# Kernel optimization log

Hardware: AMD Instinct MI355X
Metric: run time of the kernel (lower is better)

The kernel has to match this reference:

```python
import jax, jax.numpy as jnp
import numpy as np

N = 50000      # nodes
E = 800000     # edges (avg degree 16)
IN_DIM = 128
H = 4          # attention heads
D = 32         # hidden dim per head
NEG_SLOPE = 0.2


def setup_inputs() -> dict:
    key = jax.random.key(0)
    ks = jax.random.split(key, 9)
    x = jax.random.normal(ks[0], (N, IN_DIM), dtype=jnp.float32)
    src = jax.random.randint(ks[1], (E,), 0, N, dtype=jnp.int64)
    dst = jax.random.randint(ks[2], (E,), 0, N, dtype=jnp.int64)
    # layer 0: IN_DIM -> H*D ; layer 1: H*D -> H*D
    s0 = 1.0 / np.sqrt(IN_DIM)
    s1 = 1.0 / np.sqrt(H * D)
    W1 = jax.random.normal(ks[3], (H * D, IN_DIM), dtype=jnp.float32) * s0
    al1 = jax.random.normal(ks[4], (1, H, D), dtype=jnp.float32) * s1
    ar1 = jax.random.normal(ks[5], (1, H, D), dtype=jnp.float32) * s1
    W2 = jax.random.normal(ks[6], (H * D, H * D), dtype=jnp.float32) * s1
    al2 = jax.random.normal(ks[7], (1, H, D), dtype=jnp.float32) * s1
    ar2 = jax.random.normal(ks[8], (1, H, D), dtype=jnp.float32) * s1
    return {"x": x, "src": src, "dst": dst, "W1": W1, "al1": al1, "ar1": ar1,
            "W2": W2, "al2": al2, "ar2": ar2}


def gat_conv(h, src, dst, W, al, ar):
    """DGL-style GATConv. h: [N, F_in] -> [N, H, D], with ELU activation."""
    feat = (h @ W.T).reshape(N, H, D)                 # [N,H,D]
    el = jnp.sum(feat * al, axis=-1)                  # [N,H] a_l . Wh
    er = jnp.sum(feat * ar, axis=-1)                  # [N,H] a_r . Wh
    e = jax.nn.leaky_relu(el[src] + er[dst], NEG_SLOPE)  # [E,H]
    # numerically stable edge softmax over incoming edges of each dst node
    m = jax.ops.segment_max(e, dst, num_segments=N)   # [N,H]
    ee = jnp.exp(e - m[dst])                          # [E,H]
    denom = jax.ops.segment_sum(ee, dst, num_segments=N)  # [N,H]
    alpha = ee / denom[dst]                           # [E,H]
    msg = feat[src] * alpha[..., None]                # [E,H,D]
    out = jax.ops.segment_sum(msg, dst, num_segments=N)   # [N,H,D]
    return jax.nn.elu(out)


def reference(x, src, dst, W1, al1, ar1, W2, al2, ar2):
    h = gat_conv(x, src, dst, W1, al1, ar1).reshape(N, H * D)  # flatten(1)
    h = gat_conv(h, src, dst, W2, al2, ar2)                    # [N,H,D]
    return jnp.mean(h, axis=1)                                 # [N,D]
```

## Files before the change

### kernel.cpp

```cpp
#include <hip/hip_runtime.h>
#include <cmath>
#include <type_traits>

#define HEADS 4
#define FDIM 128
#define NEG 0.2f
#define NBUCK 8

typedef __attribute__((ext_vector_type(8))) __bf16 bf16x8;
typedef __attribute__((ext_vector_type(8))) _Float16 h16x8;
typedef __attribute__((ext_vector_type(4))) float f32x4;

__global__ __launch_bounds__(256) void prep_kernel(
    const float* __restrict__ W1, const float* __restrict__ al1,
    const float* __restrict__ ar1,
    const float* __restrict__ W2, const float* __restrict__ al2,
    const float* __restrict__ ar2,
    __bf16* __restrict__ wf1, __bf16* __restrict__ wext1,
    __bf16* __restrict__ wf2, __bf16* __restrict__ wext2)
{
    const int b = blockIdx.x, tid = threadIdx.x;
    if (b < 256) {
        const float* W = (b < 128) ? W1 : W2;
        __bf16* wf = (b < 128) ? wf1 : wf2;
        int idx = (b & 127) * 256 + tid;
        int j = idx & 7;
        int r = idx >> 3;
        int c = r & 15; r >>= 4;
        int t = r & 7;  r >>= 3;
        int kq = r & 15;
        int hl = r >> 4;
        float v = W[(t * 16 + c) * 128 + kq * 8 + j];
        __bf16 hi = (__bf16)v;
        wf[idx] = (hl == 0) ? hi : (__bf16)(v - (float)hi);
    } else {
        const float* W  = (b == 256) ? W1 : W2;
        const float* al = (b == 256) ? al1 : al2;
        const float* ar = (b == 256) ? ar1 : ar2;
        __bf16* wext = (b == 256) ? wext1 : wext2;
        __shared__ float val[1024];
        #pragma unroll
        for (int ch = 0; ch < 4; ++ch) {
            int idx = ch * 256 + tid;
            int c = idx >> 7, k = idx & 127;
            int h = c & 3;
            const float* a = (c < 4) ? al : ar;
            float s = 0.f;
            for (int d = 0; d < 32; ++d)
                s += a[h * 32 + d] * W[(h * 32 + d) * 128 + k];
            val[c * 128 + k] = s;
        }
        __syncthreads();
        #pragma unroll
        for (int ch = 0; ch < 16; ++ch) {
            int idx = tid * 16 + ch;
            int j = idx & 7;
            int r = idx >> 3;
            int c = r & 15; r >>= 4;
            int kq = r & 15;
            int hl = r >> 4;
            float v = (c < 8) ? val[c * 128 + kq * 8 + j] : 0.f;
            __bf16 hi = (__bf16)v;
            wext[idx] = (hl == 0) ? hi : (__bf16)(v - (float)hi);
        }
    }
}

template <typename XT>
__global__ __launch_bounds__(256) void gemm_mfma_kernel(
    const XT* __restrict__ X, const bf16x8* __restrict__ wf,
    const bf16x8* __restrict__ wext,
    _Float16* __restrict__ featH,
    float* __restrict__ el, float* __restrict__ er,
    int nnodes, int ntiles)
{
    __shared__ bf16x8 lw[4096];
    const int tid = threadIdx.x;
    for (int i = tid; i < 4096; i += 256) lw[i] = wf[i];
    __syncthreads();

    const int wave = tid >> 6, lane = tid & 63;
    const int l15 = lane & 15, quad = lane >> 4;

    int tile = blockIdx.x;
    float xr[32], xn[32];

    auto loadX = [&](int tl, float* dst) {
        int nodeA = tl * 64 + wave * 16 + l15;
        bool v = nodeA < nnodes;
        if constexpr (std::is_same<XT, float>::value) {
            const float4* xp = (const float4*)(X + (size_t)nodeA * 128);
            #pragma unroll
            for (int ks = 0; ks < 4; ++ks) {
                float4 a = v ? xp[ks * 8 + quad * 2]     : make_float4(0.f, 0.f, 0.f, 0.f);
                float4 b = v ? xp[ks * 8 + quad * 2 + 1] : make_float4(0.f, 0.f, 0.f, 0.f);
                dst[ks * 8 + 0] = a.x; dst[ks * 8 + 1] = a.y;
                dst[ks * 8 + 2] = a.z; dst[ks * 8 + 3] = a.w;
                dst[ks * 8 + 4] = b.x; dst[ks * 8 + 5] = b.y;
                dst[ks * 8 + 6] = b.z; dst[ks * 8 + 7] = b.w;
            }
        } else {
            const h16x8* xp = (const h16x8*)(X + (size_t)nodeA * 128);
            #pragma unroll
            for (int ks = 0; ks < 4; ++ks) {
                h16x8 hv;
                if (v) {
                    hv = xp[ks * 4 + quad];
                } else {
                    #pragma unroll
                    for (int j = 0; j < 8; ++j) hv[j] = (_Float16)0.f;
                }
                #pragma unroll
                for (int j = 0; j < 8; ++j) dst[ks * 8 + j] = (float)hv[j];
            }
        }
    };

    loadX(tile, xr);
    while (true) {
        int next = tile + gridDim.x;
        if (next < ntiles) loadX(next, xn);

        f32x4 acc[9];
        #pragma unroll
        for (int t = 0; t < 9; ++t) acc[t] = (f32x4){0.f, 0.f, 0.f, 0.f};

        #pragma unroll
        for (int ks = 0; ks < 4; ++ks) {
            bf16x8 ahi, alo;
            #pragma unroll
            for (int j = 0; j < 8; ++j) {
                float xv = xr[ks * 8 + j];
                __bf16 h = (__bf16)xv;
                ahi[j] = h;
                alo[j] = (__bf16)(xv - (float)h);
            }
            const int kq = ks * 4 + quad;

            {
                bf16x8 bh = wext[(kq) * 16 + l15];
                bf16x8 bl = wext[(16 + kq) * 16 + l15];
                acc[8] = __builtin_amdgcn_mfma_f32_16x16x32_bf16(ahi, bh, acc[8], 0, 0, 0);
                acc[8] = __builtin_amdgcn_mfma_f32_16x16x32_bf16(alo, bh, acc[8], 0, 0, 0);
                acc[8] = __builtin_amdgcn_mfma_f32_16x16x32_bf16(ahi, bl, acc[8], 0, 0, 0);
            }
            #pragma unroll
            for (int t = 0; t < 8; ++t) {
                bf16x8 bh = lw[(kq * 8 + t) * 16 + l15];
                bf16x8 bl = lw[((16 + kq) * 8 + t) * 16 + l15];
                acc[t] = __builtin_amdgcn_mfma_f32_16x16x32_bf16(ahi, bh, acc[t], 0, 0, 0);
                acc[t] = __builtin_amdgcn_mfma_f32_16x16x32_bf16(alo, bh, acc[t], 0, 0, 0);
                acc[t] = __builtin_amdgcn_mfma_f32_16x16x32_bf16(ahi, bl, acc[t], 0, 0, 0);
            }
        }

        const int nodeC = tile * 64 + wave * 16 + quad * 4;
        #pragma unroll
        for (int r = 0; r < 4; ++r) {
            int gn = nodeC + r;
            if (gn < nnodes) {
                #pragma unroll
                for (int t = 0; t < 8; ++t)
                    featH[(size_t)gn * 128 + t * 16 + l15] = (_Float16)acc[t][r];
            }
        }
        if (l15 < 8) {
            #pragma unroll
            for (int r = 0; r < 4; ++r) {
                int gn = nodeC + r;
                if (gn < nnodes) {
                    if (l15 < 4) el[gn * HEADS + l15] = acc[8][r];
                    else         er[gn * HEADS + (l15 - 4)] = acc[8][r];
                }
            }
        }

        if (next >= ntiles) break;
        #pragma unroll
        for (int i = 0; i < 32; ++i) xr[i] = xn[i];
        tile = next;
    }
}

__global__ __launch_bounds__(256) void hist_kernel(
    const int* __restrict__ src, const int* __restrict__ dst,
    int* __restrict__ counts, int* __restrict__ rank, int nedges, int shift)
{
    int i0 = (blockIdx.x * 256 + threadIdx.x) * 4;
    if (i0 + 3 < nedges) {
        int4 d = *(const int4*)&dst[i0];
        int4 s = *(const int4*)&src[i0];
        int4 r;
        r.x = atomicAdd(&counts[d.x * NBUCK + (s.x >> shift)], 1);
        r.y = atomicAdd(&counts[d.y * NBUCK + (s.y >> shift)], 1);
        r.z = atomicAdd(&counts[d.z * NBUCK + (s.z >> shift)], 1);
        r.w = atomicAdd(&counts[d.w * NBUCK + (s.w >> shift)], 1);
        *(int4*)&rank[i0] = r;
    } else {
        for (int i = i0; i < nedges; ++i)
            rank[i] = atomicAdd(&counts[dst[i] * NBUCK + (src[i] >> shift)], 1);
    }
}

__global__ __launch_bounds__(256) void scan1_kernel(
    const int* __restrict__ counts, int* __restrict__ offsets,
    int* __restrict__ bsums, int n)
{
    __shared__ int wsums[4];
    const int tid = threadIdx.x, lane = tid & 63, w = tid >> 6;
    const int i = blockIdx.x * 1024 + tid * 4;

    int4 v = make_int4(0, 0, 0, 0);
    if (i + 3 < n) v = *(const int4*)&counts[i];
    else {
        if (i < n)     v.x = counts[i];
        if (i + 1 < n) v.y = counts[i + 1];
        if (i + 2 < n) v.z = counts[i + 2];
    }
    int s0 = v.x, s1 = s0 + v.y, s2 = s1 + v.z, s3 = s2 + v.w;

    int x = s3;
    #pragma unroll
    for (int off = 1; off < 64; off <<= 1) {
        int t = __shfl_up(x, off, 64);
        if (lane >= off) x += t;
    }
    if (lane == 63) wsums[w] = x;
    __syncthreads();
    int wbase = 0;
    #pragma unroll
    for (int k = 0; k < 4; ++k) if (k < w) wbase += wsums[k];

    int tbase = wbase + x - s3;
    if (i < n)     offsets[i]     = tbase;
    if (i + 1 < n) offsets[i + 1] = tbase + s0;
    if (i + 2 < n) offsets[i + 2] = tbase + s1;
    if (i + 3 < n) offsets[i + 3] = tbase + s2;
    if (tid == 255) bsums[blockIdx.x] = wbase + x;
}

__global__ __launch_bounds__(64) void scan2_kernel(int* __restrict__ bsums, int nb)
{
    const int lane = threadIdx.x;
    int run = 0;
    for (int base = 0; base < nb; base += 64) {
        int i = base + lane;
        int v = (i < nb) ? bsums[i] : 0;
        int x = v;
        #pragma unroll
        for (int off = 1; off < 64; off <<= 1) {
            int t = __shfl_up(x, off, 64);
            if (lane >= off) x += t;
        }
        if (i < nb) bsums[i] = run + x - v;
        run += __shfl(x, 63, 64);
    }
}

__global__ __launch_bounds__(256) void scan3_kernel(
    int* __restrict__ offsets, const int* __restrict__ bsums, int n, int nedges)
{
    const int i = blockIdx.x * 1024 + threadIdx.x * 4;
    const int base = bsums[blockIdx.x];
    #pragma unroll
    for (int k = 0; k < 4; ++k)
        if (i + k < n) offsets[i + k] += base;
    if (blockIdx.x == 0 && threadIdx.x == 0) offsets[n] = nedges;
}

__global__ __launch_bounds__(256) void scatter_kernel(
    const int* __restrict__ src, const int* __restrict__ dst,
    const int* __restrict__ rank, const int* __restrict__ offsets,
    int* __restrict__ csr_src, int nedges, int shift)
{
    int i0 = (blockIdx.x * 256 + threadIdx.x) * 4;
    if (i0 + 3 < nedges) {
        int4 d = *(const int4*)&dst[i0];
        int4 r = *(const int4*)&rank[i0];
        int4 s = *(const int4*)&src[i0];
        csr_src[offsets[d.x * NBUCK + (s.x >> shift)] + r.x] = s.x;
        csr_src[offsets[d.y * NBUCK + (s.y >> shift)] + r.y] = s.y;
        csr_src[offsets[d.z * NBUCK + (s.z >> shift)] + r.z] = s.z;
        csr_src[offsets[d.w * NBUCK + (s.w >> shift)] + r.w] = s.w;
    } else {
        for (int i = i0; i < nedges; ++i)
            csr_src[offsets[dst[i] * NBUCK + (src[i] >> shift)] + rank[i]] = src[i];
    }
}

template <bool MEAN>
__global__ __launch_bounds__(256) void aggregate_kernel(
    const _Float16* __restrict__ featH, const float* __restrict__ el,
    const float* __restrict__ er, const int* __restrict__ offsets,
    const int* __restrict__ csr_src, void* __restrict__ outp, int nnodes)
{
    const int wid = (blockIdx.x * 256 + threadIdx.x) >> 6;
    const int lane = threadIdx.x & 63;
    const int g = lane >> 4, u = lane & 15, h = u >> 2;
    const int n = wid * 4 + g;
    const bool nv = n < nnodes;

    int beg = 0, end = 0;
    float ern = 0.f;
    if (nv) {
        beg = offsets[n * NBUCK];
        end = offsets[n * NBUCK + NBUCK];
        ern = er[n * HEADS + h];
    }
    int md = end - beg;
    md = max(md, __shfl_xor(md, 16, 64));
    md = max(md, __shfl_xor(md, 32, 64));

    float a[8];
    #pragma unroll
    for (int p = 0; p < 8; ++p) a[p] = 0.f;
    float sw = 0.f;

    int j = beg;
    bool v = j < end;
    int s = v ? csr_src[j] : 0;
    float q = el[s * HEADS + h];
    h16x8 f = ((const h16x8*)(featH + (size_t)s * 128))[u];

    for (int it = 0; it < md; ++it) {
        int jn = j + 1;
        bool vn = jn < end;
        int sn = vn ? csr_src[jn] : 0;
        float qn = el[sn * HEADS + h];
        h16x8 fn = ((const h16x8*)(featH + (size_t)sn * 128))[u];

        float e = q + ern;
        e = e > 0.f ? e : NEG * e;
        float w = v ? __expf(e) : 0.f;
        #pragma unroll
        for (int p = 0; p < 8; ++p) a[p] += w * (float)f[p];
        sw += w;

        j = jn; v = vn; q = qn; f = fn;
    }

    float inv = sw > 0.f ? 1.f / sw : 0.f;
    float r[8];
    #pragma unroll
    for (int p = 0; p < 8; ++p) {
        float t = a[p] * inv;
        r[p] = t > 0.f ? t : expm1f(t);
    }

    if (!MEAN) {
        if (nv) {
            h16x8 o;
            #pragma unroll
            for (int p = 0; p < 8; ++p) o[p] = (_Float16)r[p];
            ((h16x8*)outp)[(size_t)n * 16 + u] = o;
        }
    } else {
        #pragma unroll
        for (int p = 0; p < 8; ++p) {
            r[p] += __shfl_xor(r[p], 4, 64);
            r[p] += __shfl_xor(r[p], 8, 64);
        }
        if (nv && u < 4) {
            float* out = (float*)outp;
            float4* o4 = (float4*)(out + (size_t)n * 32 + u * 8);
            o4[0] = make_float4(0.25f * r[0], 0.25f * r[1], 0.25f * r[2], 0.25f * r[3]);
            o4[1] = make_float4(0.25f * r[4], 0.25f * r[5], 0.25f * r[6], 0.25f * r[7]);
        }
    }
}

extern "C" void kernel_launch(void* const* d_in, const int* in_sizes, int n_in,
                              void* d_out, int out_size, void* d_ws, size_t ws_size,
                              hipStream_t stream)
{
    const float* x   = (const float*)d_in[0];
    const int*   src = (const int*)d_in[1];
    const int*   dst = (const int*)d_in[2];
    const float* W1  = (const float*)d_in[3];
    const float* al1 = (const float*)d_in[4];
    const float* ar1 = (const float*)d_in[5];
    const float* W2  = (const float*)d_in[6];
    const float* al2 = (const float*)d_in[7];
    const float* ar2 = (const float*)d_in[8];

    const int N = in_sizes[0] / FDIM;
    const int E = in_sizes[1];
    const int NB = N * NBUCK;

    int shift = 0;
    while (((N - 1) >> shift) > (NBUCK - 1)) ++shift;

    _Float16* h1 = (_Float16*)d_ws;
    _Float16* featH = h1 + (size_t)N * FDIM;
    float* el = (float*)(featH + (size_t)N * FDIM);
    float* er = el + (size_t)N * HEADS;
    int* counts  = (int*)(er + (size_t)N * HEADS);
    int* offsets = counts + NB;
    int* rank    = offsets + (NB + 1);
    int* csr_src = rank + E;
    int* bsums   = csr_src + E;
    uintptr_t wp = ((uintptr_t)(bsums + 512) + 63) & ~(uintptr_t)63;
    __bf16* wf1   = (__bf16*)wp;
    __bf16* wext1 = wf1 + 32768;
    __bf16* wf2   = wext1 + 4096;
    __bf16* wext2 = wf2 + 32768;

    const int ntiles = (N + 63) / 64;
    const int gemm_grid = ntiles < 256 ? ntiles : 256;
    const int edge4_grid = ((E + 3) / 4 + 255) / 256;
    const int agg_grid  = ((N + 3) / 4 + 3) / 4;
    const int nscan     = (NB + 1023) / 1024;

    prep_kernel<<<258, 256, 0, stream>>>(W1, al1, ar1, W2, al2, ar2,
                                         wf1, wext1, wf2, wext2);

    (void)hipMemsetAsync(counts, 0, (size_t)NB * sizeof(int), stream);
    hist_kernel<<<edge4_grid, 256, 0, stream>>>(src, dst, counts, rank, E, shift);
    scan1_kernel<<<nscan, 256, 0, stream>>>(counts, offsets, bsums, NB);
    scan2_kernel<<<1, 64, 0, stream>>>(bsums, nscan);
    scan3_kernel<<<nscan, 256, 0, stream>>>(offsets, bsums, NB, E);
    scatter_kernel<<<edge4_grid, 256, 0, stream>>>(src, dst, rank, offsets,
                                                   csr_src, E, shift);

    gemm_mfma_kernel<float><<<gemm_grid, 256, 0, stream>>>(
        x, (const bf16x8*)wf1, (const bf16x8*)wext1, featH, el, er, N, ntiles);
    aggregate_kernel<false><<<agg_grid, 256, 0, stream>>>(
        featH, el, er, offsets, csr_src, (void*)h1, N);

    gemm_mfma_kernel<_Float16><<<gemm_grid, 256, 0, stream>>>(
        h1, (const bf16x8*)wf2, (const bf16x8*)wext2, featH, el, er, N, ntiles);
    aggregate_kernel<true><<<agg_grid, 256, 0, stream>>>(
        featH, el, er, offsets, csr_src, d_out, N);
}
```

Baseline: 250.0 us.

## Split each node's edges across a wave, fuse memset and scan stages

The aggregate kernel now assigns one 64-lane wave per destination node. Its four 16-lane groups stride over the node's edges and combine partial sums with cross-lane shuffles, where previously each group handled its own node for as many iterations as the longest of the four. Zeroing the histogram counts is folded into extra prep_kernel blocks in place of a memset. The single-block scan2 and scan3 kernels are merged so that each block sums the preceding block totals itself. The intent is to remove load imbalance from varying degrees and cut two launches, at the cost of four times as many aggregate waves and extra shuffle reductions.

```diff
diff --git a/kernel.cpp b/kernel.cpp
--- a/kernel.cpp
+++ b/kernel.cpp
@@ -17,7 +17,8 @@
     const float* __restrict__ W2, const float* __restrict__ al2,
     const float* __restrict__ ar2,
     __bf16* __restrict__ wf1, __bf16* __restrict__ wext1,
-    __bf16* __restrict__ wf2, __bf16* __restrict__ wext2)
+    __bf16* __restrict__ wf2, __bf16* __restrict__ wext2,
+    int* __restrict__ counts, int nb)
 {
     const int b = blockIdx.x, tid = threadIdx.x;
     if (b < 256) {
@@ -33,7 +34,7 @@
         float v = W[(t * 16 + c) * 128 + kq * 8 + j];
         __bf16 hi = (__bf16)v;
         wf[idx] = (hl == 0) ? hi : (__bf16)(v - (float)hi);
-    } else {
+    } else if (b < 258) {
         const float* W  = (b == 256) ? W1 : W2;
         const float* al = (b == 256) ? al1 : al2;
         const float* ar = (b == 256) ? ar1 : ar2;
@@ -62,6 +63,13 @@
             float v = (c < 8) ? val[c * 128 + kq * 8 + j] : 0.f;
             __bf16 hi = (__bf16)v;
             wext[idx] = (hl == 0) ? hi : (__bf16)(v - (float)hi);
+        }
+    } else {
+        int i0 = ((b - 258) * 256 + tid) * 4;
+        if (i0 + 3 < nb) {
+            *(int4*)&counts[i0] = make_int4(0, 0, 0, 0);
+        } else {
+            for (int i = i0; i < nb; ++i) counts[i] = 0;
         }
     }
 }
@@ -239,33 +247,25 @@
     if (tid == 255) bsums[blockIdx.x] = wbase + x;
 }
 
-__global__ __launch_bounds__(64) void scan2_kernel(int* __restrict__ bsums, int nb)
-{
-    const int lane = threadIdx.x;
-    int run = 0;
-    for (int base = 0; base < nb; base += 64) {
-        int i = base + lane;
-        int v = (i < nb) ? bsums[i] : 0;
-        int x = v;
-        #pragma unroll
-        for (int off = 1; off < 64; off <<= 1) {
-            int t = __shfl_up(x, off, 64);
-            if (lane >= off) x += t;
-        }
-        if (i < nb) bsums[i] = run + x - v;
-        run += __shfl(x, 63, 64);
-    }
-}
-
-__global__ __launch_bounds__(256) void scan3_kernel(
+__global__ __launch_bounds__(256) void scan23_kernel(
     int* __restrict__ offsets, const int* __restrict__ bsums, int n, int nedges)
 {
-    const int i = blockIdx.x * 1024 + threadIdx.x * 4;
-    const int base = bsums[blockIdx.x];
+    __shared__ int sbase;
+    const int tid = threadIdx.x, b = blockIdx.x;
+    if (tid < 64) {
+        int s = 0;
+        for (int i = tid; i < b; i += 64) s += bsums[i];
+        #pragma unroll
+        for (int off = 1; off < 64; off <<= 1) s += __shfl_xor(s, off, 64);
+        if (tid == 0) sbase = s;
+    }
+    __syncthreads();
+    const int base = sbase;
+    const int i = b * 1024 + tid * 4;
     #pragma unroll
     for (int k = 0; k < 4; ++k)
         if (i + k < n) offsets[i + k] += base;
-    if (blockIdx.x == 0 && threadIdx.x == 0) offsets[n] = nedges;
+    if (b == 0 && tid == 0) offsets[n] = nedges;
 }
 
 __global__ __launch_bounds__(256) void scatter_kernel(
@@ -294,36 +294,27 @@
     const float* __restrict__ er, const int* __restrict__ offsets,
     const int* __restrict__ csr_src, void* __restrict__ outp, int nnodes)
 {
-    const int wid = (blockIdx.x * 256 + threadIdx.x) >> 6;
+    const int n = (blockIdx.x * 256 + threadIdx.x) >> 6;
+    if (n >= nnodes) return;
     const int lane = threadIdx.x & 63;
     const int g = lane >> 4, u = lane & 15, h = u >> 2;
-    const int n = wid * 4 + g;
-    const bool nv = n < nnodes;
-
-    int beg = 0, end = 0;
-    float ern = 0.f;
-    if (nv) {
-        beg = offsets[n * NBUCK];
-        end = offsets[n * NBUCK + NBUCK];
-        ern = er[n * HEADS + h];
-    }
-    int md = end - beg;
-    md = max(md, __shfl_xor(md, 16, 64));
-    md = max(md, __shfl_xor(md, 32, 64));
+    const int beg = offsets[n * NBUCK], end = offsets[n * NBUCK + NBUCK];
+    const float ern = er[n * HEADS + h];
+    const int iters = (end - beg + 3) >> 2;
 
     float a[8];
     #pragma unroll
     for (int p = 0; p < 8; ++p) a[p] = 0.f;
     float sw = 0.f;
 
-    int j = beg;
+    int j = beg + g;
     bool v = j < end;
     int s = v ? csr_src[j] : 0;
     float q = el[s * HEADS + h];
     h16x8 f = ((const h16x8*)(featH + (size_t)s * 128))[u];
 
-    for (int it = 0; it < md; ++it) {
-        int jn = j + 1;
+    for (int it = 0; it < iters; ++it) {
+        int jn = j + 4;
         bool vn = jn < end;
         int sn = vn ? csr_src[jn] : 0;
         float qn = el[sn * HEADS + h];
@@ -339,6 +330,14 @@
         j = jn; v = vn; q = qn; f = fn;
     }
 
+    #pragma unroll
+    for (int p = 0; p < 8; ++p) {
+        a[p] += __shfl_xor(a[p], 16, 64);
+        a[p] += __shfl_xor(a[p], 32, 64);
+    }
+    sw += __shfl_xor(sw, 16, 64);
+    sw += __shfl_xor(sw, 32, 64);
+
     float inv = sw > 0.f ? 1.f / sw : 0.f;
     float r[8];
     #pragma unroll
@@ -348,7 +347,7 @@
     }
 
     if (!MEAN) {
-        if (nv) {
+        if (g == 0) {
             h16x8 o;
             #pragma unroll
             for (int p = 0; p < 8; ++p) o[p] = (_Float16)r[p];
@@ -360,7 +359,7 @@
             r[p] += __shfl_xor(r[p], 4, 64);
             r[p] += __shfl_xor(r[p], 8, 64);
         }
-        if (nv && u < 4) {
+        if (g == 0 && u < 4) {
             float* out = (float*)outp;
             float4* o4 = (float4*)(out + (size_t)n * 32 + u * 8);
             o4[0] = make_float4(0.25f * r[0], 0.25f * r[1], 0.25f * r[2], 0.25f * r[3]);
@@ -408,17 +407,16 @@
     const int ntiles = (N + 63) / 64;
     const int gemm_grid = ntiles < 256 ? ntiles : 256;
     const int edge4_grid = ((E + 3) / 4 + 255) / 256;
-    const int agg_grid  = ((N + 3) / 4 + 3) / 4;
+    const int agg_grid  = (N + 3) / 4;
     const int nscan     = (NB + 1023) / 1024;
-
-    prep_kernel<<<258, 256, 0, stream>>>(W1, al1, ar1, W2, al2, ar2,
-                                         wf1, wext1, wf2, wext2);
-
-    (void)hipMemsetAsync(counts, 0, (size_t)NB * sizeof(int), stream);
+    const int zblocks   = ((NB + 3) / 4 + 255) / 256;
+
+    prep_kernel<<<258 + zblocks, 256, 0, stream>>>(
+        W1, al1, ar1, W2, al2, ar2, wf1, wext1, wf2, wext2, counts, NB);
+
     hist_kernel<<<edge4_grid, 256, 0, stream>>>(src, dst, counts, rank, E, shift);
     scan1_kernel<<<nscan, 256, 0, stream>>>(counts, offsets, bsums, NB);
-    scan2_kernel<<<1, 64, 0, stream>>>(bsums, nscan);
-    scan3_kernel<<<nscan, 256, 0, stream>>>(offsets, bsums, NB, E);
+    scan23_kernel<<<nscan, 256, 0, stream>>>(offsets, bsums, NB, E);
     scatter_kernel<<<edge4_grid, 256, 0, stream>>>(src, dst, rank, offsets,
                                                    csr_src, E, shift);
 
```

New measurement: 253.6 us. No clear change (+1.4%).
